# Kernel optimization log

Hardware: AMD Instinct MI355X
Metric: run time of the kernel (lower is better)

Reference implementation:

```python
import jax, jax.numpy as jnp
import numpy as np

B, H, W, C = 8, 64, 64, 768
NH, HD = 12, 64          # num_heads, head_dim
WS = 16                  # window size
SCALE = HD ** -0.5


def setup_inputs() -> dict:
    key = jax.random.key(0)
    ks = jax.random.split(key, 6)
    x = jax.random.normal(ks[0], (B, H * W, C), dtype=jnp.float32)
    w_qkv = jax.random.normal(ks[1], (3 * C, C), dtype=jnp.float32) * 0.02
    w_out = jax.random.normal(ks[2], (C, C), dtype=jnp.float32) * 0.02
    b_out = jnp.zeros((C,), dtype=jnp.float32)
    rel_pos_h = jax.random.normal(ks[3], (2 * WS - 1, HD), dtype=jnp.float32) * 0.02
    rel_pos_w = jax.random.normal(ks[4], (2 * WS - 1, HD), dtype=jnp.float32) * 0.02
    return {"x": x, "w_qkv": w_qkv, "w_out": w_out, "b_out": b_out,
            "rel_pos_h": rel_pos_h, "rel_pos_w": rel_pos_w}


def reference(x, w_qkv, w_out, b_out, rel_pos_h, rel_pos_w):
    nh_w, nw_w = H // WS, W // WS
    xw = x.reshape(B, nh_w, WS, nw_w, WS, C).transpose(0, 1, 3, 2, 4, 5)
    Bw = B * nh_w * nw_w
    t = WS * WS
    xw = xw.reshape(Bw, t, C)

    # ---- qkv projection (no bias) and rearrange 'b t (qkv l d) -> qkv b l t d'
    qkv = (xw @ w_qkv.T).reshape(Bw, t, 3, NH, HD).transpose(2, 0, 3, 1, 4)
    q, k, v = qkv[0], qkv[1], qkv[2]        # each (Bw, NH, t, HD)

    # ---- scaled attention scores
    att = jnp.einsum('bhxd,bhyd->bhxy', q, k) * SCALE   # (Bw, NH, t, t)

    # ---- decomposed relative position bias (SAM/MViT style, q_size == k_size == WS)
    idx = jnp.arange(WS)[:, None] - jnp.arange(WS)[None, :] + (WS - 1)  # (WS, WS)
    Rh = rel_pos_h[idx]                      # (WS, WS, HD)
    Rw = rel_pos_w[idx]                      # (WS, WS, HD)
    rq = q.reshape(Bw * NH, WS, WS, HD)
    rel_h = jnp.einsum('bhwc,hkc->bhwk', rq, Rh)   # (Bw*NH, WS, WS, WS)
    rel_w = jnp.einsum('bhwc,wkc->bhwk', rq, Rw)
    att = (att.reshape(Bw * NH, WS, WS, WS, WS)
           + rel_h[:, :, :, :, None]
           + rel_w[:, :, :, None, :]).reshape(Bw, NH, t, t)

    # ---- softmax + AV
    att = jax.nn.softmax(att, axis=-1)
    o = jnp.einsum('bhxy,bhyd->bhxd', att, v)          # (Bw, NH, t, HD)
    o = o.transpose(0, 2, 1, 3).reshape(Bw, t, C)      # 'b h l d -> b l (h d)'

    # ---- output projection
    o = o @ w_out.T + b_out

    # ---- window unpartition back to (B, H*W, C)
    o = o.reshape(B, nh_w, nw_w, WS, WS, C).transpose(0, 1, 3, 2, 4, 5)
    return o.reshape(B, H * W, C)
```

## Files before the change

kernel.cpp:

```cpp
#include <hip/hip_runtime.h>

typedef __attribute__((ext_vector_type(8))) short bf16x8;
typedef __attribute__((ext_vector_type(4))) float f32x4;
typedef unsigned short u16;

__device__ __forceinline__ u16 f2bf(float f) {
  union { float f; unsigned u; } v; v.f = f;
  unsigned r = v.u + 0x7fffu + ((v.u >> 16) & 1u);
  return (u16)(r >> 16);
}
__device__ __forceinline__ float bf2f(u16 u) {
  union { unsigned u; float f; } v; v.u = ((unsigned)u) << 16;
  return v.f;
}
__device__ __forceinline__ void gload16(const void* g, void* l) {
  __builtin_amdgcn_global_load_lds((const __attribute__((address_space(1))) void*)g,
                                   (__attribute__((address_space(3))) void*)l, 16, 0, 0);
}

__global__ void sab_cvt_kernel(const float* __restrict__ src, u16* __restrict__ dst, int n4) {
  int i = blockIdx.x * blockDim.x + threadIdx.x;
  if (i >= n4) return;
  float4 f = reinterpret_cast<const float4*>(src)[i];
  ushort4 o; o.x = f2bf(f.x); o.y = f2bf(f.y); o.z = f2bf(f.z); o.w = f2bf(f.w);
  reinterpret_cast<ushort4*>(dst)[i] = o;
}

__global__ void sab_xw_kernel(const float* __restrict__ x, u16* __restrict__ xw) {
  const int r = blockIdx.x;
  const int w = r >> 8, tt = r & 255;
  const int b = w >> 4, h1 = (w >> 2) & 3, w1 = w & 3;
  const int i = tt >> 4, j = tt & 15;
  const long xrow = (long)b * 4096 + (h1 * 16 + i) * 64 + w1 * 16 + j;
  const float4* src = reinterpret_cast<const float4*>(x + xrow * 768);
  ushort4* dst = reinterpret_cast<ushort4*>(xw + (long)r * 768);
  const int c = threadIdx.x;
  float4 f = src[c];
  ushort4 o; o.x = f2bf(f.x); o.y = f2bf(f.y); o.z = f2bf(f.z); o.w = f2bf(f.w);
  dst[c] = o;
}

template<int EPI>
__global__ __launch_bounds__(256, 2)
void sab_gemm_kernel(const u16* __restrict__ A, const u16* __restrict__ Bt,
                     u16* __restrict__ outB, float* __restrict__ outF,
                     const float* __restrict__ bias, const int K, const int N)
{
  __shared__ __align__(16) u16 Ash[128 * 64];
  __shared__ __align__(16) u16 Bsh[128 * 64];
  const int tid = threadIdx.x;
  const int lane = tid & 63, wid = tid >> 6;
  const int wr = wid >> 1, wc = wid & 1;
  const int lr = lane & 15, lg = lane >> 4;
  const long m0 = (long)blockIdx.x * 128;
  const long n0 = (long)blockIdx.y * 128;

  const int srow = tid >> 3;
  const int scol = (tid & 7) * 8;
  const u16* Ag = A + (m0 + srow) * K + scol;
  const u16* Bg = Bt + (n0 + srow) * K + scol;
  u16* Al = Ash + wid * 512;
  u16* Bl = Bsh + wid * 512;

  f32x4 acc[4][4];
#pragma unroll
  for (int a = 0; a < 4; ++a)
#pragma unroll
    for (int b = 0; b < 4; ++b) acc[a][b] = (f32x4){0.f, 0.f, 0.f, 0.f};

  for (int kt = 0; kt < K; kt += 64) {
#pragma unroll
    for (int i = 0; i < 4; ++i) {
      gload16(Ag + (long)i * 32 * K + kt, Al + i * 2048);
      gload16(Bg + (long)i * 32 * K + kt, Bl + i * 2048);
    }
    __syncthreads();
    bf16x8 af[4][2], bfr[4][2];
#pragma unroll
    for (int mt = 0; mt < 4; ++mt)
#pragma unroll
      for (int kc = 0; kc < 2; ++kc)
        af[mt][kc] = *reinterpret_cast<const bf16x8*>(&Ash[(wr * 64 + mt * 16 + lr) * 64 + kc * 32 + lg * 8]);
#pragma unroll
    for (int nt = 0; nt < 4; ++nt)
#pragma unroll
      for (int kc = 0; kc < 2; ++kc)
        bfr[nt][kc] = *reinterpret_cast<const bf16x8*>(&Bsh[(wc * 64 + nt * 16 + lr) * 64 + kc * 32 + lg * 8]);
#pragma unroll
    for (int kc = 0; kc < 2; ++kc)
#pragma unroll
      for (int mt = 0; mt < 4; ++mt)
#pragma unroll
        for (int nt = 0; nt < 4; ++nt)
          acc[mt][nt] = __builtin_amdgcn_mfma_f32_16x16x32_bf16(af[mt][kc], bfr[nt][kc], acc[mt][nt], 0, 0, 0);
    __syncthreads();
  }

#pragma unroll
  for (int mt = 0; mt < 4; ++mt)
#pragma unroll
    for (int nt = 0; nt < 4; ++nt) {
      const long col = n0 + wc * 64 + nt * 16 + lr;
      float bv = 0.f;
      if (EPI == 1) bv = bias[col];
#pragma unroll
      for (int r = 0; r < 4; ++r) {
        const long row = m0 + wr * 64 + mt * 16 + lg * 4 + r;
        if (EPI == 0) {
          outB[row * N + col] = f2bf(acc[mt][nt][r]);
        } else {
          const int rr = (int)row;
          const int w = rr >> 8, tt = rr & 255;
          const long xrow = (long)(w >> 4) * 4096 + (((w >> 2) & 3) * 16 + (tt >> 4)) * 64 + (w & 3) * 16 + (tt & 15);
          outF[xrow * 768 + col] = acc[mt][nt][r] + bv;
        }
      }
    }
}

__global__ __launch_bounds__(256, 2)
void sab_attn_kernel(const u16* __restrict__ qkv, const float* __restrict__ rph,
                     const float* __restrict__ rpw, u16* __restrict__ oatt)
{
  __shared__ __align__(16) u16 relh_s[256 * 16];
  __shared__ __align__(16) u16 relw_s[256 * 16];
  __shared__ __align__(16) u16 VT[64 * 80];
  __shared__ __align__(16) u16 Sbuf[4][64 * 72];

  const int blk = blockIdx.x;
  const int w = blk / 12, h = blk % 12;
  const long qbase = (long)w * 256;
  const int tid = threadIdx.x, lane = tid & 63, wid = tid >> 6;
  const int lr = lane & 15, lg = lane >> 4;

  const u16* Qp = qkv + (long)h * 64;
  const u16* Kp = qkv + 768 + (long)h * 64;
  const u16* Vp = qkv + 1536 + (long)h * 64;

#pragma unroll
  for (int ii = 0; ii < 4; ++ii) {
    const int i = wid * 4 + ii;
    f32x4 acc = (f32x4){0.f, 0.f, 0.f, 0.f};
#pragma unroll
    for (int kc = 0; kc < 2; ++kc) {
      bf16x8 a = *reinterpret_cast<const bf16x8*>(&Qp[(qbase + i * 16 + lr) * 2304 + kc * 32 + lg * 8]);
      const float* bp = rph + (i - lr + 15) * 64 + kc * 32 + lg * 8;
      bf16x8 b;
#pragma unroll
      for (int e = 0; e < 8; ++e) b[e] = (short)f2bf(bp[e]);
      acc = __builtin_amdgcn_mfma_f32_16x16x32_bf16(a, b, acc, 0, 0, 0);
    }
#pragma unroll
    for (int r = 0; r < 4; ++r)
      relh_s[(i * 16 + lg * 4 + r) * 16 + lr] = f2bf(acc[r]);
  }
#pragma unroll
  for (int jj = 0; jj < 4; ++jj) {
    const int j = wid * 4 + jj;
    f32x4 acc = (f32x4){0.f, 0.f, 0.f, 0.f};
#pragma unroll
    for (int kc = 0; kc < 2; ++kc) {
      bf16x8 a = *reinterpret_cast<const bf16x8*>(&Qp[(qbase + lr * 16 + j) * 2304 + kc * 32 + lg * 8]);
      const float* bp = rpw + (j - lr + 15) * 64 + kc * 32 + lg * 8;
      bf16x8 b;
#pragma unroll
      for (int e = 0; e < 8; ++e) b[e] = (short)f2bf(bp[e]);
      acc = __builtin_amdgcn_mfma_f32_16x16x32_bf16(a, b, acc, 0, 0, 0);
    }
#pragma unroll
    for (int r = 0; r < 4; ++r)
      relw_s[((lg * 4 + r) * 16 + j) * 16 + lr] = f2bf(acc[r]);
  }
  __syncthreads();

  bf16x8 qa[4][2];
#pragma unroll
  for (int mt = 0; mt < 4; ++mt)
#pragma unroll
    for (int kc = 0; kc < 2; ++kc)
      qa[mt][kc] = *reinterpret_cast<const bf16x8*>(&Qp[(qbase + wid * 64 + mt * 16 + lr) * 2304 + kc * 32 + lg * 8]);

  float rw[4][4];
#pragma unroll
  for (int mt = 0; mt < 4; ++mt)
#pragma unroll
    for (int r = 0; r < 4; ++r)
      rw[mt][r] = bf2f(relw_s[(wid * 64 + mt * 16 + lg * 4 + r) * 16 + lr]);

  float mrun[4][4], lrun[4][4];
  f32x4 oacc[4][4];
#pragma unroll
  for (int mt = 0; mt < 4; ++mt)
#pragma unroll
    for (int r = 0; r < 4; ++r) { mrun[mt][r] = -1e30f; lrun[mt][r] = 0.f; }
#pragma unroll
  for (int mt = 0; mt < 4; ++mt)
#pragma unroll
    for (int nt = 0; nt < 4; ++nt) oacc[mt][nt] = (f32x4){0.f, 0.f, 0.f, 0.f};

  u16* sb = &Sbuf[wid][0];

  for (int kb = 0; kb < 4; ++kb) {
    __syncthreads();
    {
      const int key = tid >> 2, d0 = (tid & 3) * 16;
      const u16* vs = &Vp[(qbase + kb * 64 + key) * 2304 + d0];
      bf16x8 v0 = *reinterpret_cast<const bf16x8*>(vs);
      bf16x8 v1 = *reinterpret_cast<const bf16x8*>(vs + 8);
#pragma unroll
      for (int e = 0; e < 8; ++e) VT[(d0 + e) * 80 + key] = (u16)v0[e];
#pragma unroll
      for (int e = 0; e < 8; ++e) VT[(d0 + 8 + e) * 80 + key] = (u16)v1[e];
    }
    __syncthreads();

    bf16x8 kf[4][2];
#pragma unroll
    for (int nt = 0; nt < 4; ++nt)
#pragma unroll
      for (int kc = 0; kc < 2; ++kc)
        kf[nt][kc] = *reinterpret_cast<const bf16x8*>(&Kp[(qbase + kb * 64 + nt * 16 + lr) * 2304 + kc * 32 + lg * 8]);
    f32x4 s[4][4];
#pragma unroll
    for (int mt = 0; mt < 4; ++mt)
#pragma unroll
      for (int nt = 0; nt < 4; ++nt) {
        f32x4 t = (f32x4){0.f, 0.f, 0.f, 0.f};
#pragma unroll
        for (int kc = 0; kc < 2; ++kc)
          t = __builtin_amdgcn_mfma_f32_16x16x32_bf16(qa[mt][kc], kf[nt][kc], t, 0, 0, 0);
        s[mt][nt] = t;
      }

#pragma unroll
    for (int mt = 0; mt < 4; ++mt) {
      float sv[4][4];
#pragma unroll
      for (int r = 0; r < 4; ++r) {
        const int x = wid * 64 + mt * 16 + lg * 4 + r;
#pragma unroll
        for (int nt = 0; nt < 4; ++nt)
          sv[r][nt] = s[mt][nt][r] * 0.125f + bf2f(relh_s[x * 16 + kb * 4 + nt]) + rw[mt][r];
      }
#pragma unroll
      for (int r = 0; r < 4; ++r) {
        float rmax = fmaxf(fmaxf(sv[r][0], sv[r][1]), fmaxf(sv[r][2], sv[r][3]));
        rmax = fmaxf(rmax, __shfl_xor(rmax, 1));
        rmax = fmaxf(rmax, __shfl_xor(rmax, 2));
        rmax = fmaxf(rmax, __shfl_xor(rmax, 4));
        rmax = fmaxf(rmax, __shfl_xor(rmax, 8));
        const float mnew = fmaxf(mrun[mt][r], rmax);
        const float sf = __expf(mrun[mt][r] - mnew);
        mrun[mt][r] = mnew;
        float rsum = 0.f;
#pragma unroll
        for (int nt = 0; nt < 4; ++nt) { const float p = __expf(sv[r][nt] - mnew); sv[r][nt] = p; rsum += p; }
        rsum += __shfl_xor(rsum, 1);
        rsum += __shfl_xor(rsum, 2);
        rsum += __shfl_xor(rsum, 4);
        rsum += __shfl_xor(rsum, 8);
        lrun[mt][r] = lrun[mt][r] * sf + rsum;
#pragma unroll
        for (int nt = 0; nt < 4; ++nt) oacc[mt][nt][r] *= sf;
        const int rowl = mt * 16 + lg * 4 + r;
#pragma unroll
        for (int nt = 0; nt < 4; ++nt) sb[rowl * 72 + nt * 16 + lr] = f2bf(sv[r][nt]);
      }
    }
    __syncthreads();

#pragma unroll
    for (int kc = 0; kc < 2; ++kc) {
      bf16x8 vf[4];
#pragma unroll
      for (int nt = 0; nt < 4; ++nt)
        vf[nt] = *reinterpret_cast<const bf16x8*>(&VT[(nt * 16 + lr) * 80 + kc * 32 + lg * 8]);
#pragma unroll
      for (int mt = 0; mt < 4; ++mt) {
        bf16x8 pa = *reinterpret_cast<const bf16x8*>(&sb[(mt * 16 + lr) * 72 + kc * 32 + lg * 8]);
#pragma unroll
        for (int nt = 0; nt < 4; ++nt)
          oacc[mt][nt] = __builtin_amdgcn_mfma_f32_16x16x32_bf16(pa, vf[nt], oacc[mt][nt], 0, 0, 0);
      }
    }
  }

#pragma unroll
  for (int mt = 0; mt < 4; ++mt)
#pragma unroll
    for (int r = 0; r < 4; ++r) {
      const float inv = 1.f / lrun[mt][r];
      const long row = qbase + wid * 64 + mt * 16 + lg * 4 + r;
#pragma unroll
      for (int nt = 0; nt < 4; ++nt)
        oatt[row * 768 + h * 64 + nt * 16 + lr] = f2bf(oacc[mt][nt][r] * inv);
    }
}

extern "C" void kernel_launch(void* const* d_in, const int* in_sizes, int n_in,
                              void* d_out, int out_size, void* d_ws, size_t ws_size,
                              hipStream_t stream) {
  (void)in_sizes; (void)n_in; (void)out_size; (void)ws_size;
  const float* x     = (const float*)d_in[0];
  const float* w_qkv = (const float*)d_in[1];
  const float* w_out = (const float*)d_in[2];
  const float* b_out = (const float*)d_in[3];
  const float* rph   = (const float*)d_in[4];
  const float* rpw   = (const float*)d_in[5];
  float* out = (float*)d_out;

  char* ws = (char*)d_ws;
  u16* qkv   = (u16*)ws;
  u16* xw    = (u16*)(ws + 150994944L);
  u16* wqkvb = (u16*)(ws + 201326592L);
  u16* woutb = (u16*)(ws + 204865536L);
  u16* oatt  = xw;

  sab_cvt_kernel<<<dim3(1728), dim3(256), 0, stream>>>(w_qkv, wqkvb, 442368);
  sab_cvt_kernel<<<dim3(576), dim3(256), 0, stream>>>(w_out, woutb, 147456);
  sab_xw_kernel<<<dim3(32768), dim3(192), 0, stream>>>(x, xw);
  sab_gemm_kernel<0><<<dim3(256, 18), dim3(256), 0, stream>>>(xw, wqkvb, qkv, nullptr, nullptr, 768, 2304);
  sab_attn_kernel<<<dim3(1536), dim3(256), 0, stream>>>(qkv, rph, rpw, oatt);
  sab_gemm_kernel<1><<<dim3(256, 6), dim3(256), 0, stream>>>(oatt, woutb, nullptr, out, b_out, 768, 768);
}
```

Measured before the change: 371.1 us.

## Write V transposed from QKV GEMM epilogue and drop LDS V transpose in attention

The QKV GEMM epilogue now writes Q/K into a 1536-wide buffer and V into a separate transposed layout (head-dim major, token contiguous). The attention kernel then loads V fragments directly from global memory, removing the per-block LDS transpose and two of the block-wide barriers per key block. Other changes: the GEMM launch bound rises to 4 blocks per SM, attention blocks are remapped with a swizzle, and the score computation is interleaved per row tile. The transposed V stores are strided 8-byte writes, which may be less efficient, and the barrier removal relies on each wave using only its own Sbuf region.

```diff
diff --git a/kernel.cpp b/kernel.cpp
--- a/kernel.cpp
+++ b/kernel.cpp
@@ -41,10 +41,11 @@
 }
 
 template<int EPI>
-__global__ __launch_bounds__(256, 2)
+__global__ __launch_bounds__(256, 4)
 void sab_gemm_kernel(const u16* __restrict__ A, const u16* __restrict__ Bt,
-                     u16* __restrict__ outB, float* __restrict__ outF,
-                     const float* __restrict__ bias, const int K, const int N)
+                     u16* __restrict__ outB, u16* __restrict__ vTp,
+                     float* __restrict__ outF, const float* __restrict__ bias,
+                     const int K, const int N)
 {
   __shared__ __align__(16) u16 Ash[128 * 64];
   __shared__ __align__(16) u16 Bsh[128 * 64];
@@ -101,15 +102,23 @@
 #pragma unroll
     for (int nt = 0; nt < 4; ++nt) {
       const long col = n0 + wc * 64 + nt * 16 + lr;
-      float bv = 0.f;
-      if (EPI == 1) bv = bias[col];
-#pragma unroll
-      for (int r = 0; r < 4; ++r) {
-        const long row = m0 + wr * 64 + mt * 16 + lg * 4 + r;
-        if (EPI == 0) {
-          outB[row * N + col] = f2bf(acc[mt][nt][r]);
+      if (EPI == 0) {
+        const long row0 = m0 + wr * 64 + mt * 16 + lg * 4;
+        if (n0 < 1536) {
+#pragma unroll
+          for (int r = 0; r < 4; ++r)
+            outB[(row0 + r) * 1536 + col] = f2bf(acc[mt][nt][r]);
         } else {
-          const int rr = (int)row;
+          ushort4 o;
+          o.x = f2bf(acc[mt][nt][0]); o.y = f2bf(acc[mt][nt][1]);
+          o.z = f2bf(acc[mt][nt][2]); o.w = f2bf(acc[mt][nt][3]);
+          *reinterpret_cast<ushort4*>(&vTp[(col - 1536) * 32768L + row0]) = o;
+        }
+      } else {
+        const float bv = bias[col];
+#pragma unroll
+        for (int r = 0; r < 4; ++r) {
+          const int rr = (int)(m0 + wr * 64 + mt * 16 + lg * 4 + r);
           const int w = rr >> 8, tt = rr & 255;
           const long xrow = (long)(w >> 4) * 4096 + (((w >> 2) & 3) * 16 + (tt >> 4)) * 64 + (w & 3) * 16 + (tt & 15);
           outF[xrow * 768 + col] = acc[mt][nt][r] + bv;
@@ -119,23 +128,24 @@
 }
 
 __global__ __launch_bounds__(256, 2)
-void sab_attn_kernel(const u16* __restrict__ qkv, const float* __restrict__ rph,
-                     const float* __restrict__ rpw, u16* __restrict__ oatt)
+void sab_attn_kernel(const u16* __restrict__ qk, const u16* __restrict__ vT,
+                     const float* __restrict__ rph, const float* __restrict__ rpw,
+                     u16* __restrict__ oatt)
 {
   __shared__ __align__(16) u16 relh_s[256 * 16];
   __shared__ __align__(16) u16 relw_s[256 * 16];
-  __shared__ __align__(16) u16 VT[64 * 80];
   __shared__ __align__(16) u16 Sbuf[4][64 * 72];
 
-  const int blk = blockIdx.x;
+  const int blk0 = blockIdx.x;
+  const int blk = (blk0 & 7) * 192 + (blk0 >> 3);
   const int w = blk / 12, h = blk % 12;
   const long qbase = (long)w * 256;
   const int tid = threadIdx.x, lane = tid & 63, wid = tid >> 6;
   const int lr = lane & 15, lg = lane >> 4;
 
-  const u16* Qp = qkv + (long)h * 64;
-  const u16* Kp = qkv + 768 + (long)h * 64;
-  const u16* Vp = qkv + 1536 + (long)h * 64;
+  const u16* Qp = qk + (long)h * 64;
+  const u16* Kp = qk + 768 + (long)h * 64;
+  const u16* Vt = vT + (long)h * 64 * 32768 + w * 256;
 
 #pragma unroll
   for (int ii = 0; ii < 4; ++ii) {
@@ -143,7 +153,7 @@
     f32x4 acc = (f32x4){0.f, 0.f, 0.f, 0.f};
 #pragma unroll
     for (int kc = 0; kc < 2; ++kc) {
-      bf16x8 a = *reinterpret_cast<const bf16x8*>(&Qp[(qbase + i * 16 + lr) * 2304 + kc * 32 + lg * 8]);
+      bf16x8 a = *reinterpret_cast<const bf16x8*>(&Qp[(qbase + i * 16 + lr) * 1536 + kc * 32 + lg * 8]);
       const float* bp = rph + (i - lr + 15) * 64 + kc * 32 + lg * 8;
       bf16x8 b;
 #pragma unroll
@@ -160,7 +170,7 @@
     f32x4 acc = (f32x4){0.f, 0.f, 0.f, 0.f};
 #pragma unroll
     for (int kc = 0; kc < 2; ++kc) {
-      bf16x8 a = *reinterpret_cast<const bf16x8*>(&Qp[(qbase + lr * 16 + j) * 2304 + kc * 32 + lg * 8]);
+      bf16x8 a = *reinterpret_cast<const bf16x8*>(&Qp[(qbase + lr * 16 + j) * 1536 + kc * 32 + lg * 8]);
       const float* bp = rpw + (j - lr + 15) * 64 + kc * 32 + lg * 8;
       bf16x8 b;
 #pragma unroll
@@ -178,7 +188,7 @@
   for (int mt = 0; mt < 4; ++mt)
 #pragma unroll
     for (int kc = 0; kc < 2; ++kc)
-      qa[mt][kc] = *reinterpret_cast<const bf16x8*>(&Qp[(qbase + wid * 64 + mt * 16 + lr) * 2304 + kc * 32 + lg * 8]);
+      qa[mt][kc] = *reinterpret_cast<const bf16x8*>(&Qp[(qbase + wid * 64 + mt * 16 + lr) * 1536 + kc * 32 + lg * 8]);
 
   float rw[4][4];
 #pragma unroll
@@ -201,50 +211,34 @@
   u16* sb = &Sbuf[wid][0];
 
   for (int kb = 0; kb < 4; ++kb) {
-    __syncthreads();
-    {
-      const int key = tid >> 2, d0 = (tid & 3) * 16;
-      const u16* vs = &Vp[(qbase + kb * 64 + key) * 2304 + d0];
-      bf16x8 v0 = *reinterpret_cast<const bf16x8*>(vs);
-      bf16x8 v1 = *reinterpret_cast<const bf16x8*>(vs + 8);
-#pragma unroll
-      for (int e = 0; e < 8; ++e) VT[(d0 + e) * 80 + key] = (u16)v0[e];
-#pragma unroll
-      for (int e = 0; e < 8; ++e) VT[(d0 + 8 + e) * 80 + key] = (u16)v1[e];
-    }
-    __syncthreads();
-
-    bf16x8 kf[4][2];
+    bf16x8 kf[4][2], vf[4][2];
 #pragma unroll
     for (int nt = 0; nt < 4; ++nt)
 #pragma unroll
-      for (int kc = 0; kc < 2; ++kc)
-        kf[nt][kc] = *reinterpret_cast<const bf16x8*>(&Kp[(qbase + kb * 64 + nt * 16 + lr) * 2304 + kc * 32 + lg * 8]);
-    f32x4 s[4][4];
-#pragma unroll
-    for (int mt = 0; mt < 4; ++mt)
+      for (int kc = 0; kc < 2; ++kc) {
+        kf[nt][kc] = *reinterpret_cast<const bf16x8*>(&Kp[(qbase + kb * 64 + nt * 16 + lr) * 1536 + kc * 32 + lg * 8]);
+        vf[nt][kc] = *reinterpret_cast<const bf16x8*>(&Vt[(nt * 16 + lr) * 32768L + kb * 64 + kc * 32 + lg * 8]);
+      }
+
+#pragma unroll
+    for (int mt = 0; mt < 4; ++mt) {
+      f32x4 sn[4];
 #pragma unroll
       for (int nt = 0; nt < 4; ++nt) {
         f32x4 t = (f32x4){0.f, 0.f, 0.f, 0.f};
 #pragma unroll
         for (int kc = 0; kc < 2; ++kc)
           t = __builtin_amdgcn_mfma_f32_16x16x32_bf16(qa[mt][kc], kf[nt][kc], t, 0, 0, 0);
-        s[mt][nt] = t;
-      }
-
-#pragma unroll
-    for (int mt = 0; mt < 4; ++mt) {
-      float sv[4][4];
+        sn[nt] = t;
+      }
 #pragma unroll
       for (int r = 0; r < 4; ++r) {
         const int x = wid * 64 + mt * 16 + lg * 4 + r;
+        float sv[4];
 #pragma unroll
         for (int nt = 0; nt < 4; ++nt)
-          sv[r][nt] = s[mt][nt][r] * 0.125f + bf2f(relh_s[x * 16 + kb * 4 + nt]) + rw[mt][r];
-      }
-#pragma unroll
-      for (int r = 0; r < 4; ++r) {
-        float rmax = fmaxf(fmaxf(sv[r][0], sv[r][1]), fmaxf(sv[r][2], sv[r][3]));
+          sv[nt] = sn[nt][r] * 0.125f + bf2f(relh_s[x * 16 + kb * 4 + nt]) + rw[mt][r];
+        float rmax = fmaxf(fmaxf(sv[0], sv[1]), fmaxf(sv[2], sv[3]));
         rmax = fmaxf(rmax, __shfl_xor(rmax, 1));
         rmax = fmaxf(rmax, __shfl_xor(rmax, 2));
         rmax = fmaxf(rmax, __shfl_xor(rmax, 4));
@@ -254,7 +248,7 @@
         mrun[mt][r] = mnew;
         float rsum = 0.f;
 #pragma unroll
-        for (int nt = 0; nt < 4; ++nt) { const float p = __expf(sv[r][nt] - mnew); sv[r][nt] = p; rsum += p; }
+        for (int nt = 0; nt < 4; ++nt) { const float p = __expf(sv[nt] - mnew); sv[nt] = p; rsum += p; }
         rsum += __shfl_xor(rsum, 1);
         rsum += __shfl_xor(rsum, 2);
         rsum += __shfl_xor(rsum, 4);
@@ -264,25 +258,19 @@
         for (int nt = 0; nt < 4; ++nt) oacc[mt][nt][r] *= sf;
         const int rowl = mt * 16 + lg * 4 + r;
 #pragma unroll
-        for (int nt = 0; nt < 4; ++nt) sb[rowl * 72 + nt * 16 + lr] = f2bf(sv[r][nt]);
-      }
-    }
-    __syncthreads();
-
-#pragma unroll
-    for (int kc = 0; kc < 2; ++kc) {
-      bf16x8 vf[4];
-#pragma unroll
-      for (int nt = 0; nt < 4; ++nt)
-        vf[nt] = *reinterpret_cast<const bf16x8*>(&VT[(nt * 16 + lr) * 80 + kc * 32 + lg * 8]);
+        for (int nt = 0; nt < 4; ++nt) sb[rowl * 72 + nt * 16 + lr] = f2bf(sv[nt]);
+      }
+    }
+
+#pragma unroll
+    for (int kc = 0; kc < 2; ++kc)
 #pragma unroll
       for (int mt = 0; mt < 4; ++mt) {
         bf16x8 pa = *reinterpret_cast<const bf16x8*>(&sb[(mt * 16 + lr) * 72 + kc * 32 + lg * 8]);
 #pragma unroll
         for (int nt = 0; nt < 4; ++nt)
-          oacc[mt][nt] = __builtin_amdgcn_mfma_f32_16x16x32_bf16(pa, vf[nt], oacc[mt][nt], 0, 0, 0);
-      }
-    }
+          oacc[mt][nt] = __builtin_amdgcn_mfma_f32_16x16x32_bf16(pa, vf[nt][kc], oacc[mt][nt], 0, 0, 0);
+      }
   }
 
 #pragma unroll
@@ -310,7 +298,8 @@
   float* out = (float*)d_out;
 
   char* ws = (char*)d_ws;
-  u16* qkv   = (u16*)ws;
+  u16* qk    = (u16*)ws;
+  u16* vT    = (u16*)(ws + 100663296L);
   u16* xw    = (u16*)(ws + 150994944L);
   u16* wqkvb = (u16*)(ws + 201326592L);
   u16* woutb = (u16*)(ws + 204865536L);
@@ -319,7 +308,7 @@
   sab_cvt_kernel<<<dim3(1728), dim3(256), 0, stream>>>(w_qkv, wqkvb, 442368);
   sab_cvt_kernel<<<dim3(576), dim3(256), 0, stream>>>(w_out, woutb, 147456);
   sab_xw_kernel<<<dim3(32768), dim3(192), 0, stream>>>(x, xw);
-  sab_gemm_kernel<0><<<dim3(256, 18), dim3(256), 0, stream>>>(xw, wqkvb, qkv, nullptr, nullptr, 768, 2304);
-  sab_attn_kernel<<<dim3(1536), dim3(256), 0, stream>>>(qkv, rph, rpw, oatt);
-  sab_gemm_kernel<1><<<dim3(256, 6), dim3(256), 0, stream>>>(oatt, woutb, nullptr, out, b_out, 768, 768);
-}
+  sab_gemm_kernel<0><<<dim3(256, 18), dim3(256), 0, stream>>>(xw, wqkvb, qk, vT, nullptr, nullptr, 768, 2304);
+  sab_attn_kernel<<<dim3(1536), dim3(256), 0, stream>>>(qk, vT, rph, rpw, oatt);
+  sab_gemm_kernel<1><<<dim3(256, 6), dim3(256), 0, stream>>>(oatt, woutb, nullptr, nullptr, out, b_out, 768, 768);
+}
```

After: 366.4 us. Within noise of the previous version (-1.3%).
